# Kernel tuning notes

Hardware: AMD Instinct MI355X
Metric: run time of the kernel (lower is better)

Reference implementation:

```python
import jax, jax.numpy as jnp
import numpy as np

N = 50000       # num_of_nodes
IN = 256        # in_features
HID = 128       # hidden_features
HEADS = 4       # num_of_heads
E = 800000      # num edges
ALPHA = 0.2     # leaky relu slope
EPS = 1e-6      # layernorm eps
SCALE = float(np.sqrt(HID * HEADS))


def setup_inputs() -> dict:
    key = jax.random.key(0)
    ks = jax.random.split(key, 8)
    data = jax.random.normal(ks[0], (N, IN), dtype=jnp.float32)
    edge = jax.random.randint(ks[1], (2, E), 0, N, dtype=jnp.int64)
    embed_table = jax.random.normal(ks[2], (N, IN), dtype=jnp.float32)
    # per-head Linear(in -> hidden): weight [HEADS, HID, IN], bias [HEADS, HID]
    W = jax.random.normal(ks[3], (HEADS, HID, IN), dtype=jnp.float32) / np.sqrt(IN)
    b = jax.random.normal(ks[4], (HEADS, HID), dtype=jnp.float32) * 0.01
    # attention vectors a: torch.rand -> uniform [0,1)
    a_attn = jax.random.uniform(ks[5], (HEADS, 2 * HID), dtype=jnp.float32)
    ln_gain = jnp.ones((HEADS * HID,), dtype=jnp.float32)
    ln_bias = jnp.zeros((HEADS * HID,), dtype=jnp.float32)
    return {"data": data, "edge": edge, "embed_table": embed_table,
            "W": W, "b": b, "a_attn": a_attn,
            "ln_gain": ln_gain, "ln_bias": ln_bias}


def _leaky(x):
    return jnp.where(x >= 0, x, ALPHA * x)


def reference(data, edge, embed_table, W, b, a_attn, ln_gain, ln_bias):
    # concat=True: input `data` is ignored, nodes come from embedding table
    emb = embed_table.at[0].set(0.0)  # padding_idx=0
    src, dst = edge[0], edge[1]
    heads_out = []
    for h in range(HEADS):  # small fixed head loop
        x = emb @ W[h].T + b[h]                      # [N, HID]
        # score_e = a . [x_src ; x_dst] split into per-node projections
        s1 = x @ a_attn[h, :HID]                     # [N]
        s2 = x @ a_attn[h, HID:]                     # [N]
        e = jnp.exp(_leaky(s1[src] + s2[dst]) / SCALE)   # [E]
        rowsum = jax.ops.segment_sum(e, src, num_segments=N)          # [N]
        agg = jax.ops.segment_sum(e[:, None] * x[dst], src, num_segments=N)  # [N, HID]
        denom = jnp.where(rowsum == 0, 1.0, rowsum)[:, None]
        heads_out.append(agg / denom)
    h_prime = jnp.concatenate(heads_out, axis=1)     # [N, HEADS*HID]
    # LayerNorm with torch unbiased std and (std + eps)
    mean = h_prime.mean(-1, keepdims=True)
    std = jnp.std(h_prime, axis=-1, ddof=1, keepdims=True)
    normed = ln_gain * (h_prime - mean) / (std + EPS) + ln_bias
    return jax.nn.elu(normed)
```

## Files before the change

### kernel.cpp

```cpp
#include <hip/hip_runtime.h>
#include <math.h>

#define N_NODES 50000
#define IN_F    256
#define HID     128
#define HEADS   4
#define NE      800000
#define ALPHA   0.2f
#define LN_EPS  1e-6f
#define OUT_F   512
#define INV_SCALE 0.04419417382415922f

typedef __attribute__((ext_vector_type(8))) short bf16x8;
typedef __attribute__((ext_vector_type(4))) float f32x4;

static __device__ __forceinline__ unsigned short f2bf(float f) {
  unsigned int u = __float_as_uint(f);
  unsigned int r = (u + 0x7FFFu + ((u >> 16) & 1u)) >> 16;
  return (unsigned short)r;
}
static __device__ __forceinline__ float bf2f(unsigned short h) {
  return __uint_as_float(((unsigned int)h) << 16);
}

__global__ __launch_bounds__(256) void conv_kernel(const float* __restrict__ in,
    unsigned short* __restrict__ out, int n4, int zero_first64)
{
  int i = blockIdx.x * 256 + threadIdx.x;
  if (i >= n4) return;
  float4 v = ((const float4*)in)[i];
  if (zero_first64 && i < 64) v = make_float4(0.f, 0.f, 0.f, 0.f);
  ushort4 o;
  o.x = f2bf(v.x); o.y = f2bf(v.y); o.z = f2bf(v.z); o.w = f2bf(v.w);
  ((ushort4*)out)[i] = o;
}

__global__ __launch_bounds__(256, 2) void gemm_fused(
    const unsigned short* __restrict__ embB, const unsigned short* __restrict__ WB,
    const float* __restrict__ bias, const float* __restrict__ a_attn,
    unsigned short* __restrict__ X, float* __restrict__ sbuf, int M)
{
  __shared__ unsigned short Wl[32 * 512];
  __shared__ unsigned short Al[4 * 512];
  const int tid = threadIdx.x;
  const int w = tid >> 6, lane = tid & 63;
  const int r = lane & 15, q = lane >> 4;
  const int bm = blockIdx.x * 64;
  f32x4 acc[8][4] = {};
  for (int k0 = 0; k0 < IN_F; k0 += 32) {
    __syncthreads();
    {
      int c = tid;
      int rr = c & 15, qq = (c >> 4) & 3, mb = c >> 6;
      int row = min(bm + mb * 16 + rr, M - 1);
      *(bf16x8*)(Al + c * 8) = *(const bf16x8*)(embB + (size_t)row * IN_F + k0 + qq * 8);
    }
    #pragma unroll
    for (int i2 = 0; i2 < 8; ++i2) {
      int c = i2 * 256 + tid;
      int rr = c & 15, qq = (c >> 4) & 3, nt = c >> 6;
      *(bf16x8*)(Wl + c * 8) = *(const bf16x8*)(WB + (size_t)(nt * 16 + rr) * IN_F + k0 + qq * 8);
    }
    __syncthreads();
    bf16x8 bfrag[4];
    #pragma unroll
    for (int mb = 0; mb < 4; ++mb)
      bfrag[mb] = *(const bf16x8*)(Al + mb * 512 + q * 128 + r * 8);
    #pragma unroll
    for (int t = 0; t < 8; ++t) {
      bf16x8 afrag = *(const bf16x8*)(Wl + (w * 8 + t) * 512 + q * 128 + r * 8);
      #pragma unroll
      for (int mb = 0; mb < 4; ++mb)
        acc[t][mb] = __builtin_amdgcn_mfma_f32_16x16x32_bf16(afrag, bfrag[mb], acc[t][mb], 0, 0, 0);
    }
  }
  const float* a1 = a_attn + w * 2 * HID;
  const float* a2 = a1 + HID;
  #pragma unroll
  for (int mb = 0; mb < 4; ++mb) {
    int m = bm + mb * 16 + r;
    float p1 = 0.f, p2 = 0.f;
    #pragma unroll
    for (int t = 0; t < 8; ++t) {
      int nloc = t * 16 + q * 4;
      int n = w * HID + nloc;
      float4 bz = *(const float4*)(bias + n);
      float x0 = acc[t][mb][0] + bz.x;
      float x1 = acc[t][mb][1] + bz.y;
      float x2 = acc[t][mb][2] + bz.z;
      float x3 = acc[t][mb][3] + bz.w;
      float4 av1 = *(const float4*)(a1 + nloc);
      float4 av2 = *(const float4*)(a2 + nloc);
      p1 += x0 * av1.x + x1 * av1.y + x2 * av1.z + x3 * av1.w;
      p2 += x0 * av2.x + x1 * av2.y + x2 * av2.z + x3 * av2.w;
      if (m < M) {
        ushort4 o = make_ushort4(f2bf(x0), f2bf(x1), f2bf(x2), f2bf(x3));
        *(ushort4*)(X + (size_t)m * OUT_F + n) = o;
      }
    }
    p1 += __shfl_xor(p1, 16, 64); p1 += __shfl_xor(p1, 32, 64);
    p2 += __shfl_xor(p2, 16, 64); p2 += __shfl_xor(p2, 32, 64);
    if (q == 0 && m < M) {
      sbuf[(size_t)m * 8 + w]     = p1;
      sbuf[(size_t)m * 8 + 4 + w] = p2;
    }
  }
}

__global__ void hist_kernel(const int* __restrict__ src, int* __restrict__ count)
{
  int i = blockIdx.x * blockDim.x + threadIdx.x;
  if (i < NE) {
    int s = min(max(src[i], 0), N_NODES - 1);
    atomicAdd(&count[s], 1);
  }
}

__global__ void scan_kernel(const int* __restrict__ count, int* __restrict__ offset,
                            int* __restrict__ cursor, int n)
{
  __shared__ int wsum[16];
  __shared__ int carry_s;
  const int tid = threadIdx.x;
  const int lane = tid & 63, wid = tid >> 6;
  if (tid == 0) carry_s = 0;
  __syncthreads();
  for (int base = 0; base < n; base += 1024) {
    int idx = base + tid;
    int v = (idx < n) ? count[idx] : 0;
    int s = v;
    #pragma unroll
    for (int off = 1; off < 64; off <<= 1) {
      int t = __shfl_up(s, off, 64);
      if (lane >= off) s += t;
    }
    if (lane == 63) wsum[wid] = s;
    __syncthreads();
    if (wid == 0) {
      int wv = (lane < 16) ? wsum[lane] : 0;
      int ss = wv;
      #pragma unroll
      for (int off = 1; off < 16; off <<= 1) {
        int t = __shfl_up(ss, off, 64);
        if (lane >= off) ss += t;
      }
      if (lane < 16) wsum[lane] = ss - wv;
    }
    __syncthreads();
    int excl = carry_s + wsum[wid] + (s - v);
    if (idx < n) { offset[idx] = excl; cursor[idx] = excl; }
    __syncthreads();
    if (tid == 1023) carry_s += wsum[15] + s;
    __syncthreads();
  }
}

__global__ void scatter_exp(const int* __restrict__ src, const int* __restrict__ dst,
                            int* __restrict__ cursor, const float* __restrict__ sbuf,
                            int* __restrict__ sdst, float4* __restrict__ ebuf)
{
  int i = blockIdx.x * blockDim.x + threadIdx.x;
  if (i >= NE) return;
  int s = min(max(src[i], 0), N_NODES - 1);
  int d = min(max(dst[i], 0), N_NODES - 1);
  int p = atomicAdd(&cursor[s], 1);
  sdst[p] = d;
  float4 s1 = *(const float4*)(sbuf + (size_t)s * 8);
  float4 s2 = *(const float4*)(sbuf + (size_t)d * 8 + 4);
  float t0 = s1.x + s2.x, t1 = s1.y + s2.y, t2 = s1.z + s2.z, t3 = s1.w + s2.w;
  float4 e;
  e.x = __expf((t0 >= 0.f ? t0 : ALPHA * t0) * INV_SCALE);
  e.y = __expf((t1 >= 0.f ? t1 : ALPHA * t1) * INV_SCALE);
  e.z = __expf((t2 >= 0.f ? t2 : ALPHA * t2) * INV_SCALE);
  e.w = __expf((t3 >= 0.f ? t3 : ALPHA * t3) * INV_SCALE);
  ebuf[p] = e;
}

__global__ __launch_bounds__(256) void attn_kernel(const unsigned short* __restrict__ X,
    const float* __restrict__ ebuf, const int* __restrict__ offset,
    const int* __restrict__ count, const int* __restrict__ sdst,
    const float* __restrict__ gain, const float* __restrict__ bias,
    float* __restrict__ out)
{
  const int tid = threadIdx.x;
  const int w = tid >> 6, lane = tid & 63;
  const int n = blockIdx.x * 4 + w;
  if (n >= N_NODES) return;
  const int h = lane >> 4;
  const int c0 = lane * 8;
  const int start = offset[n];
  const int deg = count[n];
  const unsigned short* Xc = X + c0;
  float acc[8] = {};
  float rowsum = 0.f;
  int i = 0;
  for (; i + 4 <= deg; i += 4) {
    int b = start + i;
    int d0 = sdst[b], d1 = sdst[b + 1], d2 = sdst[b + 2], d3 = sdst[b + 3];
    float e0 = ebuf[(size_t)b * 4 + h];
    float e1 = ebuf[(size_t)(b + 1) * 4 + h];
    float e2 = ebuf[(size_t)(b + 2) * 4 + h];
    float e3 = ebuf[(size_t)(b + 3) * 4 + h];
    bf16x8 x0 = *(const bf16x8*)(Xc + (size_t)d0 * OUT_F);
    bf16x8 x1 = *(const bf16x8*)(Xc + (size_t)d1 * OUT_F);
    bf16x8 x2 = *(const bf16x8*)(Xc + (size_t)d2 * OUT_F);
    bf16x8 x3 = *(const bf16x8*)(Xc + (size_t)d3 * OUT_F);
    rowsum += (e0 + e1) + (e2 + e3);
    #pragma unroll
    for (int j = 0; j < 8; ++j) {
      float s = acc[j];
      s += e0 * bf2f((unsigned short)x0[j]);
      s += e1 * bf2f((unsigned short)x1[j]);
      s += e2 * bf2f((unsigned short)x2[j]);
      s += e3 * bf2f((unsigned short)x3[j]);
      acc[j] = s;
    }
  }
  for (; i < deg; ++i) {
    int b = start + i;
    int d0 = sdst[b];
    float e0 = ebuf[(size_t)b * 4 + h];
    bf16x8 x0 = *(const bf16x8*)(Xc + (size_t)d0 * OUT_F);
    rowsum += e0;
    #pragma unroll
    for (int j = 0; j < 8; ++j)
      acc[j] += e0 * bf2f((unsigned short)x0[j]);
  }
  float inv = (rowsum == 0.f) ? 1.f : 1.f / rowsum;
  float v[8];
  float psum = 0.f, psq = 0.f;
  #pragma unroll
  for (int j = 0; j < 8; ++j) {
    v[j] = acc[j] * inv;
    psum += v[j];
    psq  += v[j] * v[j];
  }
  #pragma unroll
  for (int off = 32; off >= 1; off >>= 1) {
    psum += __shfl_xor(psum, off, 64);
    psq  += __shfl_xor(psq,  off, 64);
  }
  float mean = psum * (1.0f / OUT_F);
  float var  = fmaxf((psq - OUT_F * mean * mean) * (1.0f / (OUT_F - 1)), 0.f);
  float inv_std = 1.0f / (sqrtf(var) + LN_EPS);
  float4 g0 = *(const float4*)(gain + c0);
  float4 g1 = *(const float4*)(gain + c0 + 4);
  float4 bb0 = *(const float4*)(bias + c0);
  float4 bb1 = *(const float4*)(bias + c0 + 4);
  float gg[8] = {g0.x, g0.y, g0.z, g0.w, g1.x, g1.y, g1.z, g1.w};
  float bv[8] = {bb0.x, bb0.y, bb0.z, bb0.w, bb1.x, bb1.y, bb1.z, bb1.w};
  float o[8];
  #pragma unroll
  for (int j = 0; j < 8; ++j) {
    float nv = gg[j] * (v[j] - mean) * inv_std + bv[j];
    o[j] = nv > 0.f ? nv : expm1f(nv);
  }
  float* orow = out + (size_t)n * OUT_F + c0;
  *(float4*)(orow)     = make_float4(o[0], o[1], o[2], o[3]);
  *(float4*)(orow + 4) = make_float4(o[4], o[5], o[6], o[7]);
}

extern "C" void kernel_launch(void* const* d_in, const int* in_sizes, int n_in,
                              void* d_out, int out_size, void* d_ws, size_t ws_size,
                              hipStream_t stream)
{
  const int*   edge   = (const int*)d_in[1];
  const float* embed  = (const float*)d_in[2];
  const float* W      = (const float*)d_in[3];
  const float* b      = (const float*)d_in[4];
  const float* a_attn = (const float*)d_in[5];
  const float* ln_g   = (const float*)d_in[6];
  const float* ln_b   = (const float*)d_in[7];
  float* out = (float*)d_out;

  char* ws = (char*)d_ws;
  size_t off = 0;
  auto alloc = [&](size_t bytes) -> void* {
    void* p = ws + off;
    off = (off + bytes + 255) & ~(size_t)255;
    return p;
  };
  unsigned short* embB = (unsigned short*)alloc((size_t)N_NODES * IN_F * sizeof(unsigned short));
  unsigned short* WB   = (unsigned short*)alloc((size_t)OUT_F * IN_F * sizeof(unsigned short));
  unsigned short* X    = (unsigned short*)alloc((size_t)N_NODES * OUT_F * sizeof(unsigned short));
  float* sbuf   = (float*)alloc((size_t)N_NODES * 8 * sizeof(float));
  int*   count  = (int*)alloc((size_t)N_NODES * sizeof(int));
  int*   offs   = (int*)alloc((size_t)N_NODES * sizeof(int));
  int*   cursor = (int*)alloc((size_t)N_NODES * sizeof(int));
  int*   sdst   = (int*)alloc((size_t)NE * sizeof(int));
  float* ebuf   = (float*)alloc((size_t)NE * 4 * sizeof(float));

  const int* src = edge;
  const int* dst = edge + NE;

  (void)hipMemsetAsync(count, 0, N_NODES * sizeof(int), stream);
  hist_kernel<<<(NE + 255) / 256, 256, 0, stream>>>(src, count);
  scan_kernel<<<1, 1024, 0, stream>>>(count, offs, cursor, N_NODES);

  int n4e = N_NODES * IN_F / 4;
  conv_kernel<<<(n4e + 255) / 256, 256, 0, stream>>>(embed, embB, n4e, 1);
  int n4w = OUT_F * IN_F / 4;
  conv_kernel<<<(n4w + 255) / 256, 256, 0, stream>>>(W, WB, n4w, 0);

  gemm_fused<<<(N_NODES + 63) / 64, 256, 0, stream>>>(embB, WB, b, a_attn, X, sbuf, N_NODES);

  scatter_exp<<<(NE + 255) / 256, 256, 0, stream>>>(src, dst, cursor, sbuf, sdst,
                                                    (float4*)ebuf);

  attn_kernel<<<(N_NODES + 3) / 4, 256, 0, stream>>>(X, ebuf, offs, count, sdst,
                                                     ln_g, ln_b, out);
}
```

Measured before the change: 478.2 us.

## Fuse embedding conversion into GEMM, pack edge records, vectorize scan, unroll gather

Removes the separate fp32→bf16 embedding conversion pass: the GEMM now reads fp32 embeddings directly, zeroes padding row 0 and converts while staging to LDS. W tiles are loaded with global_load_lds. The scan reads and writes int4, scatter writes a single 32-byte record holding exp weights plus dst index, and attn reads these records with an 8-way unrolled gather and 32-bit addressing. The aim is less HBM traffic and fewer kernel launches. The cost is that the GEMM now reads twice the bytes for the A operand on every K step.

```diff
diff --git a/kernel.cpp b/kernel.cpp
--- a/kernel.cpp
+++ b/kernel.cpp
@@ -24,19 +24,18 @@
 }
 
 __global__ __launch_bounds__(256) void conv_kernel(const float* __restrict__ in,
-    unsigned short* __restrict__ out, int n4, int zero_first64)
+    unsigned short* __restrict__ out, int n4)
 {
   int i = blockIdx.x * 256 + threadIdx.x;
   if (i >= n4) return;
   float4 v = ((const float4*)in)[i];
-  if (zero_first64 && i < 64) v = make_float4(0.f, 0.f, 0.f, 0.f);
   ushort4 o;
   o.x = f2bf(v.x); o.y = f2bf(v.y); o.z = f2bf(v.z); o.w = f2bf(v.w);
   ((ushort4*)out)[i] = o;
 }
 
 __global__ __launch_bounds__(256, 2) void gemm_fused(
-    const unsigned short* __restrict__ embB, const unsigned short* __restrict__ WB,
+    const float* __restrict__ embF, const unsigned short* __restrict__ WB,
     const float* __restrict__ bias, const float* __restrict__ a_attn,
     unsigned short* __restrict__ X, float* __restrict__ sbuf, int M)
 {
@@ -49,17 +48,27 @@
   f32x4 acc[8][4] = {};
   for (int k0 = 0; k0 < IN_F; k0 += 32) {
     __syncthreads();
+    #pragma unroll
+    for (int i2 = 0; i2 < 8; ++i2) {
+      int c = i2 * 256 + tid;
+      int rr = c & 15, qq = (c >> 4) & 3, nt = c >> 6;
+      const unsigned short* gp = WB + (size_t)(nt * 16 + rr) * IN_F + k0 + qq * 8;
+      __builtin_amdgcn_global_load_lds(
+          (const __attribute__((address_space(1))) void*)gp,
+          (__attribute__((address_space(3))) void*)(Wl + c * 8), 16, 0, 0);
+    }
     {
       int c = tid;
       int rr = c & 15, qq = (c >> 4) & 3, mb = c >> 6;
       int row = min(bm + mb * 16 + rr, M - 1);
-      *(bf16x8*)(Al + c * 8) = *(const bf16x8*)(embB + (size_t)row * IN_F + k0 + qq * 8);
-    }
-    #pragma unroll
-    for (int i2 = 0; i2 < 8; ++i2) {
-      int c = i2 * 256 + tid;
-      int rr = c & 15, qq = (c >> 4) & 3, nt = c >> 6;
-      *(bf16x8*)(Wl + c * 8) = *(const bf16x8*)(WB + (size_t)(nt * 16 + rr) * IN_F + k0 + qq * 8);
+      const float* ap = embF + (size_t)row * IN_F + k0 + qq * 8;
+      float4 f0 = *(const float4*)ap;
+      float4 f1 = *(const float4*)(ap + 4);
+      if (row == 0) { f0 = make_float4(0.f,0.f,0.f,0.f); f1 = make_float4(0.f,0.f,0.f,0.f); }
+      ushort4 u0 = make_ushort4(f2bf(f0.x), f2bf(f0.y), f2bf(f0.z), f2bf(f0.w));
+      ushort4 u1 = make_ushort4(f2bf(f1.x), f2bf(f1.y), f2bf(f1.z), f2bf(f1.w));
+      *(ushort4*)(Al + c * 8)     = u0;
+      *(ushort4*)(Al + c * 8 + 4) = u1;
     }
     __syncthreads();
     bf16x8 bfrag[4];
@@ -116,8 +125,8 @@
   }
 }
 
-__global__ void scan_kernel(const int* __restrict__ count, int* __restrict__ offset,
-                            int* __restrict__ cursor, int n)
+__global__ void scan_kernel(const int4* __restrict__ count4, int* __restrict__ offset,
+                            int* __restrict__ cursor, int n4)
 {
   __shared__ int wsum[16];
   __shared__ int carry_s;
@@ -125,10 +134,11 @@
   const int lane = tid & 63, wid = tid >> 6;
   if (tid == 0) carry_s = 0;
   __syncthreads();
-  for (int base = 0; base < n; base += 1024) {
+  for (int base = 0; base < n4; base += 1024) {
     int idx = base + tid;
-    int v = (idx < n) ? count[idx] : 0;
-    int s = v;
+    int4 v = (idx < n4) ? count4[idx] : make_int4(0, 0, 0, 0);
+    int tsum = v.x + v.y + v.z + v.w;
+    int s = tsum;
     #pragma unroll
     for (int off = 1; off < 64; off <<= 1) {
       int t = __shfl_up(s, off, 64);
@@ -147,8 +157,13 @@
       if (lane < 16) wsum[lane] = ss - wv;
     }
     __syncthreads();
-    int excl = carry_s + wsum[wid] + (s - v);
-    if (idx < n) { offset[idx] = excl; cursor[idx] = excl; }
+    int excl = carry_s + wsum[wid] + (s - tsum);
+    if (idx < n4) {
+      int o0 = excl, o1 = o0 + v.x, o2 = o1 + v.y, o3 = o2 + v.z;
+      int4 ov = make_int4(o0, o1, o2, o3);
+      ((int4*)offset)[idx] = ov;
+      ((int4*)cursor)[idx] = ov;
+    }
     __syncthreads();
     if (tid == 1023) carry_s += wsum[15] + s;
     __syncthreads();
@@ -157,14 +172,13 @@
 
 __global__ void scatter_exp(const int* __restrict__ src, const int* __restrict__ dst,
                             int* __restrict__ cursor, const float* __restrict__ sbuf,
-                            int* __restrict__ sdst, float4* __restrict__ ebuf)
+                            char* __restrict__ rec)
 {
   int i = blockIdx.x * blockDim.x + threadIdx.x;
   if (i >= NE) return;
   int s = min(max(src[i], 0), N_NODES - 1);
   int d = min(max(dst[i], 0), N_NODES - 1);
   int p = atomicAdd(&cursor[s], 1);
-  sdst[p] = d;
   float4 s1 = *(const float4*)(sbuf + (size_t)s * 8);
   float4 s2 = *(const float4*)(sbuf + (size_t)d * 8 + 4);
   float t0 = s1.x + s2.x, t1 = s1.y + s2.y, t2 = s1.z + s2.z, t3 = s1.w + s2.w;
@@ -173,12 +187,14 @@
   e.y = __expf((t1 >= 0.f ? t1 : ALPHA * t1) * INV_SCALE);
   e.z = __expf((t2 >= 0.f ? t2 : ALPHA * t2) * INV_SCALE);
   e.w = __expf((t3 >= 0.f ? t3 : ALPHA * t3) * INV_SCALE);
-  ebuf[p] = e;
+  char* rp = rec + (size_t)p * 32;
+  *(float4*)rp = e;
+  *(int*)(rp + 16) = d;
 }
 
 __global__ __launch_bounds__(256) void attn_kernel(const unsigned short* __restrict__ X,
-    const float* __restrict__ ebuf, const int* __restrict__ offset,
-    const int* __restrict__ count, const int* __restrict__ sdst,
+    const char* __restrict__ rec, const int* __restrict__ offset,
+    const int* __restrict__ count,
     const float* __restrict__ gain, const float* __restrict__ bias,
     float* __restrict__ out)
 {
@@ -186,26 +202,43 @@
   const int w = tid >> 6, lane = tid & 63;
   const int n = blockIdx.x * 4 + w;
   if (n >= N_NODES) return;
-  const int h = lane >> 4;
+  const int h4 = (lane >> 4) * 4;
   const int c0 = lane * 8;
+  const unsigned c0b = (unsigned)(c0 * 2);
   const int start = offset[n];
   const int deg = count[n];
-  const unsigned short* Xc = X + c0;
+  const char* Xb = (const char*)X;
+  const char* rbase = rec + (size_t)start * 32;
   float acc[8] = {};
   float rowsum = 0.f;
   int i = 0;
-  for (; i + 4 <= deg; i += 4) {
-    int b = start + i;
-    int d0 = sdst[b], d1 = sdst[b + 1], d2 = sdst[b + 2], d3 = sdst[b + 3];
-    float e0 = ebuf[(size_t)b * 4 + h];
-    float e1 = ebuf[(size_t)(b + 1) * 4 + h];
-    float e2 = ebuf[(size_t)(b + 2) * 4 + h];
-    float e3 = ebuf[(size_t)(b + 3) * 4 + h];
-    bf16x8 x0 = *(const bf16x8*)(Xc + (size_t)d0 * OUT_F);
-    bf16x8 x1 = *(const bf16x8*)(Xc + (size_t)d1 * OUT_F);
-    bf16x8 x2 = *(const bf16x8*)(Xc + (size_t)d2 * OUT_F);
-    bf16x8 x3 = *(const bf16x8*)(Xc + (size_t)d3 * OUT_F);
-    rowsum += (e0 + e1) + (e2 + e3);
+  for (; i + 8 <= deg; i += 8) {
+    const char* rb = rbase + (size_t)i * 32;
+    int d0 = *(const int*)(rb + 16);
+    int d1 = *(const int*)(rb + 48);
+    int d2 = *(const int*)(rb + 80);
+    int d3 = *(const int*)(rb + 112);
+    int d4 = *(const int*)(rb + 144);
+    int d5 = *(const int*)(rb + 176);
+    int d6 = *(const int*)(rb + 208);
+    int d7 = *(const int*)(rb + 240);
+    float e0 = *(const float*)(rb + h4);
+    float e1 = *(const float*)(rb + h4 + 32);
+    float e2 = *(const float*)(rb + h4 + 64);
+    float e3 = *(const float*)(rb + h4 + 96);
+    float e4 = *(const float*)(rb + h4 + 128);
+    float e5 = *(const float*)(rb + h4 + 160);
+    float e6 = *(const float*)(rb + h4 + 192);
+    float e7 = *(const float*)(rb + h4 + 224);
+    bf16x8 x0 = *(const bf16x8*)(Xb + (((unsigned)d0 << 10) + c0b));
+    bf16x8 x1 = *(const bf16x8*)(Xb + (((unsigned)d1 << 10) + c0b));
+    bf16x8 x2 = *(const bf16x8*)(Xb + (((unsigned)d2 << 10) + c0b));
+    bf16x8 x3 = *(const bf16x8*)(Xb + (((unsigned)d3 << 10) + c0b));
+    bf16x8 x4 = *(const bf16x8*)(Xb + (((unsigned)d4 << 10) + c0b));
+    bf16x8 x5 = *(const bf16x8*)(Xb + (((unsigned)d5 << 10) + c0b));
+    bf16x8 x6 = *(const bf16x8*)(Xb + (((unsigned)d6 << 10) + c0b));
+    bf16x8 x7 = *(const bf16x8*)(Xb + (((unsigned)d7 << 10) + c0b));
+    rowsum += ((e0 + e1) + (e2 + e3)) + ((e4 + e5) + (e6 + e7));
     #pragma unroll
     for (int j = 0; j < 8; ++j) {
       float s = acc[j];
@@ -213,14 +246,18 @@
       s += e1 * bf2f((unsigned short)x1[j]);
       s += e2 * bf2f((unsigned short)x2[j]);
       s += e3 * bf2f((unsigned short)x3[j]);
+      s += e4 * bf2f((unsigned short)x4[j]);
+      s += e5 * bf2f((unsigned short)x5[j]);
+      s += e6 * bf2f((unsigned short)x6[j]);
+      s += e7 * bf2f((unsigned short)x7[j]);
       acc[j] = s;
     }
   }
   for (; i < deg; ++i) {
-    int b = start + i;
-    int d0 = sdst[b];
-    float e0 = ebuf[(size_t)b * 4 + h];
-    bf16x8 x0 = *(const bf16x8*)(Xc + (size_t)d0 * OUT_F);
+    const char* rb = rbase + (size_t)i * 32;
+    int d0 = *(const int*)(rb + 16);
+    float e0 = *(const float*)(rb + h4);
+    bf16x8 x0 = *(const bf16x8*)(Xb + (((unsigned)d0 << 10) + c0b));
     rowsum += e0;
     #pragma unroll
     for (int j = 0; j < 8; ++j)
@@ -280,33 +317,27 @@
     off = (off + bytes + 255) & ~(size_t)255;
     return p;
   };
-  unsigned short* embB = (unsigned short*)alloc((size_t)N_NODES * IN_F * sizeof(unsigned short));
   unsigned short* WB   = (unsigned short*)alloc((size_t)OUT_F * IN_F * sizeof(unsigned short));
   unsigned short* X    = (unsigned short*)alloc((size_t)N_NODES * OUT_F * sizeof(unsigned short));
   float* sbuf   = (float*)alloc((size_t)N_NODES * 8 * sizeof(float));
   int*   count  = (int*)alloc((size_t)N_NODES * sizeof(int));
   int*   offs   = (int*)alloc((size_t)N_NODES * sizeof(int));
   int*   cursor = (int*)alloc((size_t)N_NODES * sizeof(int));
-  int*   sdst   = (int*)alloc((size_t)NE * sizeof(int));
-  float* ebuf   = (float*)alloc((size_t)NE * 4 * sizeof(float));
+  char*  rec    = (char*)alloc((size_t)NE * 32);
 
   const int* src = edge;
   const int* dst = edge + NE;
 
   (void)hipMemsetAsync(count, 0, N_NODES * sizeof(int), stream);
   hist_kernel<<<(NE + 255) / 256, 256, 0, stream>>>(src, count);
-  scan_kernel<<<1, 1024, 0, stream>>>(count, offs, cursor, N_NODES);
-
-  int n4e = N_NODES * IN_F / 4;
-  conv_kernel<<<(n4e + 255) / 256, 256, 0, stream>>>(embed, embB, n4e, 1);
+  scan_kernel<<<1, 1024, 0, stream>>>((const int4*)count, offs, cursor, N_NODES / 4);
+
   int n4w = OUT_F * IN_F / 4;
-  conv_kernel<<<(n4w + 255) / 256, 256, 0, stream>>>(W, WB, n4w, 0);
-
-  gemm_fused<<<(N_NODES + 63) / 64, 256, 0, stream>>>(embB, WB, b, a_attn, X, sbuf, N_NODES);
-
-  scatter_exp<<<(NE + 255) / 256, 256, 0, stream>>>(src, dst, cursor, sbuf, sdst,
-                                                    (float4*)ebuf);
-
-  attn_kernel<<<(N_NODES + 3) / 4, 256, 0, stream>>>(X, ebuf, offs, count, sdst,
-                                                     ln_g, ln_b, out);
-}
+  conv_kernel<<<(n4w + 255) / 256, 256, 0, stream>>>(W, WB, n4w);
+
+  gemm_fused<<<(N_NODES + 63) / 64, 256, 0, stream>>>(embed, WB, b, a_attn, X, sbuf, N_NODES);
+
+  scatter_exp<<<(NE + 255) / 256, 256, 0, stream>>>(src, dst, cursor, sbuf, rec);
+
+  attn_kernel<<<(N_NODES + 3) / 4, 256, 0, stream>>>(X, rec, offs, count, ln_g, ln_b, out);
+}
```

New measurement: 436.3 us. -8.8%, faster.
